# Kernel optimization log

Measured on AMD Instinct MI355X. Metric: run time of the kernel, lower is better.

The kernel has to match this reference:

```python
import jax, jax.numpy as jnp
import numpy as np

B = 16384   # tokens
K = 2       # top_k
E = 64      # num_experts
H = 512     # hidden_dim
F = 1024    # expert ffn dim


def setup_inputs() -> dict:
    key = jax.random.key(0)
    k1, k2, k3, k4, k5 = jax.random.split(key, 5)
    hidden_states = jax.random.normal(k1, (B, H), dtype=jnp.float32)
    expert_weights = jax.nn.softmax(jax.random.normal(k2, (B, K), dtype=jnp.float32), axis=-1)
    # Balanced routing: exactly B*K/E assignments per expert (random permutation
    # of a tiled pattern). This is a valid routing for the module and lets the
    # reference use a fixed-capacity grouped GEMM with zero token dropping.
    flat_ids = jax.random.permutation(k3, jnp.tile(jnp.arange(E, dtype=jnp.int32), (B * K) // E))
    expert_ids = flat_ids.reshape(B, K)
    W1 = jax.random.normal(k4, (E, H, F), dtype=jnp.float32) * (1.0 / np.sqrt(H))
    W2 = jax.random.normal(k5, (E, F, H), dtype=jnp.float32) * (1.0 / np.sqrt(F))
    return {"hidden_states": hidden_states, "expert_weights": expert_weights,
            "expert_ids": expert_ids, "W1": W1, "W2": W2}


def reference(hidden_states, expert_weights, expert_ids, W1, W2):
    # Faithful to ExpertGrouping.group_dispatch: every (token, slot) assignment
    # is run through its expert, scaled by its routing weight, and index_add'ed
    # back into the per-token output. Since assignments within an expert are
    # order-independent, we sort assignments by expert id and run one grouped
    # batched GEMM (the fused equivalent of the per-group/per-expert loops).
    b, h = hidden_states.shape
    k = expert_ids.shape[1]
    e = W1.shape[0]
    n = b * k
    cap = n // e  # exact per-expert count (balanced routing)

    flat_ids = expert_ids.reshape(-1)            # [N]
    flat_w = expert_weights.reshape(-1)          # [N]
    token_idx = jnp.arange(n, dtype=jnp.int32) // k  # [N] token for each assignment

    order = jnp.argsort(flat_ids)                # stable sort: groups assignments by expert
    tok_sorted = token_idx[order]                # [N]
    w_sorted = flat_w[order]                     # [N]

    # Gather-dispatch: [E, cap, H]
    xg = hidden_states[tok_sorted].reshape(e, cap, h)
    # Grouped expert FFN (batched over experts)
    hid = jax.nn.silu(jnp.einsum('ech,ehf->ecf', xg, W1))
    yg = jnp.einsum('ecf,efh->ech', hid, W2)     # [E, cap, H]

    # Weighted scatter-combine back to tokens
    weighted = yg.reshape(n, h) * w_sorted[:, None]
    out = jnp.zeros((b, h), dtype=hidden_states.dtype).at[tok_sorted].add(weighted)
    return out
```

## Files before the change

kernel.cpp:

```cpp
#include <hip/hip_runtime.h>
#include <hip/hip_bf16.h>

#define B_TOK 16384
#define TOPK 2
#define NEXP 64
#define HID 512
#define FFN 1024
#define NASSIGN (B_TOK * TOPK)
#define CAP (NASSIGN / NEXP)

typedef unsigned short u16;
typedef __bf16 bf16_t;
typedef bf16_t bf16x8 __attribute__((ext_vector_type(8)));
typedef float f32x4 __attribute__((ext_vector_type(4)));

__device__ __forceinline__ unsigned pkbf(float a, float b) {
  union { bf16_t h[2]; unsigned u; } v;
  v.h[0] = (bf16_t)a; v.h[1] = (bf16_t)b;
  return v.u;
}
__device__ __forceinline__ u16 f2bf(float f) {
  union { bf16_t h; u16 u; } v; v.h = (bf16_t)f; return v.u;
}
__device__ __forceinline__ float bf2f(unsigned u16v) {
  union { unsigned u; float f; } v; v.u = u16v << 16; return v.f;
}

#define GLOAD_LDS16(g, l)                                                     \
  __builtin_amdgcn_global_load_lds((const __attribute__((address_space(1))) void*)(g), \
                                   (__attribute__((address_space(3))) void*)(l), 16, 0, 0)

__global__ void k_route(const int* __restrict__ ids, int* __restrict__ cnt,
                        int* __restrict__ tok_of, int* __restrict__ slot_pos) {
  int n = blockIdx.x * blockDim.x + threadIdx.x;
  if (n >= NASSIGN) return;
  int e = ids[n];
  int r = atomicAdd(&cnt[e], 1);
  int p = e * CAP + r;
  tok_of[p] = n >> 1;
  slot_pos[n] = p;
}

__global__ void k_gather(const float* __restrict__ hs, const int* __restrict__ tok_of,
                         u16* __restrict__ Xg) {
  int p = blockIdx.x * 4 + (threadIdx.x >> 6);
  int lane = threadIdx.x & 63;
  const float4* src = reinterpret_cast<const float4*>(hs + (size_t)tok_of[p] * HID);
  uint2* dst = reinterpret_cast<uint2*>(Xg + (size_t)p * HID);
#pragma unroll
  for (int i = 0; i < 2; i++) {
    float4 v = src[i * 64 + lane];
    uint2 o;
    o.x = pkbf(v.x, v.y);
    o.y = pkbf(v.z, v.w);
    dst[i * 64 + lane] = o;
  }
}

template <int K, int NN, bool SILU>
__global__ __launch_bounds__(512, 2) void k_gemm(const u16* __restrict__ A,
                                                 const float* __restrict__ Wf,
                                                 u16* __restrict__ Cout) {
  constexpr int MT = CAP / 256;
  constexpr int NT = NN / 256;
  constexpr int NWG = NEXP * MT * NT;
  constexpr int Q = NWG / 8;
  constexpr int KT = K / 64;
  int wg = (blockIdx.x % 8) * Q + blockIdx.x / 8;
  int e = wg / (MT * NT);
  int rm = wg % (MT * NT);
  int mt = rm / NT, nt = rm % NT;

  const u16* Ab = A + ((size_t)e * CAP + (size_t)mt * 256) * K;

  __shared__ __align__(16) char smc[131072];

  int t_ = threadIdx.x;
  int lane = t_ & 63, wv = t_ >> 6;
  int wm = wv >> 2, wn = wv & 3;
  int l15 = lane & 15, lhi = lane >> 4;

  int srow = t_ >> 3;
  int gchunk = (t_ & 7) ^ (srow & 7);
  const u16* gA = Ab + (size_t)srow * K + gchunk * 8;
#define STAGE_HALF_A(tn, j)                                                  \
  do {                                                                       \
    char* d_ = smc + ((tn) & 1) * 32768 + (j) * 16384 + wv * 1024;           \
    const u16* s_ = gA + (size_t)((j) * 128) * K + (tn) * 64;                \
    GLOAD_LDS16(s_, d_);                                                     \
    GLOAD_LDS16(s_ + (size_t)64 * K, d_ + 8192);                             \
  } while (0)

  int kunit = t_ >> 6;
  int nunit = t_ & 63;
  const float* gWb = Wf + (size_t)e * K * NN + (size_t)(kunit * 8) * NN +
                     (size_t)nt * 256 + nunit * 4;
  int wbo[4];
#pragma unroll
  for (int i = 0; i < 4; i++) {
    int n = nunit * 4 + i;
    int S = (n ^ (n >> 3)) & 7;
    wbo[i] = n * 128 + ((kunit ^ S) << 4);
  }

  f32x4 acc[8][4];
#pragma unroll
  for (int i = 0; i < 8; i++)
#pragma unroll
    for (int j = 0; j < 4; j++) {
      f32x4 z = {0.f, 0.f, 0.f, 0.f};
      acc[i][j] = z;
    }
  bf16x8 a[4][2], b[4][2];

  int aof0 = (wm * 128 + l15) * 128 + ((lhi ^ (l15 & 7)) << 4);
  int aof1 = (wm * 128 + l15) * 128 + (((4 + lhi) ^ (l15 & 7)) << 4);
  int boff[4][2];
#pragma unroll
  for (int nf = 0; nf < 4; nf++) {
    int r = wn * 64 + nf * 16 + l15;
    int Sr = (r ^ (r >> 3)) & 7;
    boff[nf][0] = r * 128 + ((lhi ^ Sr) << 4);
    boff[nf][1] = r * 128 + (((4 + lhi) ^ Sr) << 4);
  }

#define BAR_THEN_LGKM0()                                                     \
  do {                                                                       \
    __builtin_amdgcn_sched_barrier(0);                                       \
    __builtin_amdgcn_s_barrier();                                            \
    asm volatile("s_waitcnt lgkmcnt(0)" ::: "memory");                       \
    __builtin_amdgcn_sched_barrier(0);                                       \
  } while (0)

#define MFMA_QUAD(mh, nh)                                                    \
  do {                                                                       \
    __builtin_amdgcn_s_setprio(1);                                           \
    _Pragma("unroll") for (int mf = 0; mf < 4; mf++)                         \
        _Pragma("unroll") for (int nf = 0; nf < 2; nf++)                     \
            _Pragma("unroll") for (int kk = 0; kk < 2; kk++)                 \
                acc[(mh)*4 + mf][(nh)*2 + nf] = __builtin_amdgcn_mfma_f32_16x16x32_bf16( \
                    a[mf][kk], b[(nh)*2 + nf][kk], acc[(mh)*4 + mf][(nh)*2 + nf], 0, 0, 0); \
    __builtin_amdgcn_s_setprio(0);                                           \
  } while (0)

  STAGE_HALF_A(0, 0); STAGE_HALF_A(0, 1);
  if (KT > 1) { STAGE_HALF_A(1, 0); STAGE_HALF_A(1, 1); }
  {
    float4 P[8];
#pragma unroll
    for (int j = 0; j < 8; j++)
      P[j] = *reinterpret_cast<const float4*>(gWb + (size_t)j * NN);
    char* wB = smc + 65536;
#pragma unroll
    for (int i = 0; i < 4; i++) {
      uint4 v;
      v.x = pkbf(P[0][i], P[1][i]); v.y = pkbf(P[2][i], P[3][i]);
      v.z = pkbf(P[4][i], P[5][i]); v.w = pkbf(P[6][i], P[7][i]);
      *reinterpret_cast<uint4*>(wB + wbo[i]) = v;
    }
  }
  asm volatile("s_waitcnt vmcnt(0) lgkmcnt(0)" ::: "memory");
  __builtin_amdgcn_sched_barrier(0);
  __builtin_amdgcn_s_barrier();

  for (int t = 0; t < KT; t++) {
    const char* pA = smc + (t & 1) * 32768;
    const char* pB = smc + 65536 + (t & 1) * 32768;
    char* wB = smc + 65536 + ((t + 1) & 1) * 32768;
    float4 L0, L1, L2, L3, L4, L5, L6, L7;

#pragma unroll
    for (int mf = 0; mf < 4; mf++) {
      a[mf][0] = *reinterpret_cast<const bf16x8*>(pA + aof0 + mf * 2048);
      a[mf][1] = *reinterpret_cast<const bf16x8*>(pA + aof1 + mf * 2048);
    }
#pragma unroll
    for (int nf = 0; nf < 2; nf++) {
      b[nf][0] = *reinterpret_cast<const bf16x8*>(pB + boff[nf][0]);
      b[nf][1] = *reinterpret_cast<const bf16x8*>(pB + boff[nf][1]);
    }
    if (t + 1 < KT) {
      const float* g = gWb + (size_t)(t + 1) * 64 * NN;
      L0 = *reinterpret_cast<const float4*>(g);
      L1 = *reinterpret_cast<const float4*>(g + (size_t)1 * NN);
      L2 = *reinterpret_cast<const float4*>(g + (size_t)2 * NN);
      L3 = *reinterpret_cast<const float4*>(g + (size_t)3 * NN);
    }
    BAR_THEN_LGKM0();
    MFMA_QUAD(0, 0);
    __builtin_amdgcn_s_barrier();

#pragma unroll
    for (int nf = 0; nf < 2; nf++) {
      b[2 + nf][0] = *reinterpret_cast<const bf16x8*>(pB + boff[2 + nf][0]);
      b[2 + nf][1] = *reinterpret_cast<const bf16x8*>(pB + boff[2 + nf][1]);
    }
    if (t + 1 < KT) {
      const float* g = gWb + (size_t)(t + 1) * 64 * NN;
      L4 = *reinterpret_cast<const float4*>(g + (size_t)4 * NN);
      L5 = *reinterpret_cast<const float4*>(g + (size_t)5 * NN);
      L6 = *reinterpret_cast<const float4*>(g + (size_t)6 * NN);
      L7 = *reinterpret_cast<const float4*>(g + (size_t)7 * NN);
    }
    BAR_THEN_LGKM0();
    MFMA_QUAD(0, 1);
    __builtin_amdgcn_s_barrier();

#pragma unroll
    for (int mf = 0; mf < 4; mf++) {
      a[mf][0] = *reinterpret_cast<const bf16x8*>(pA + aof0 + (4 + mf) * 2048);
      a[mf][1] = *reinterpret_cast<const bf16x8*>(pA + aof1 + (4 + mf) * 2048);
    }
    BAR_THEN_LGKM0();
    MFMA_QUAD(1, 0);
    __builtin_amdgcn_s_barrier();

    if (t + 2 < KT) { STAGE_HALF_A(t + 2, 0); STAGE_HALF_A(t + 2, 1); }
    if (t + 1 < KT) {
      if (t + 2 < KT)
        asm volatile("s_waitcnt vmcnt(4)" ::: "memory");
      else
        asm volatile("s_waitcnt vmcnt(0)" ::: "memory");
      __builtin_amdgcn_sched_barrier(0);
#pragma unroll
      for (int i = 0; i < 4; i++) {
        uint4 v;
        v.x = pkbf(L0[i], L1[i]); v.y = pkbf(L2[i], L3[i]);
        v.z = pkbf(L4[i], L5[i]); v.w = pkbf(L6[i], L7[i]);
        *reinterpret_cast<uint4*>(wB + wbo[i]) = v;
      }
    }
    BAR_THEN_LGKM0();
    MFMA_QUAD(1, 1);
    __builtin_amdgcn_s_barrier();
  }
#undef STAGE_HALF_A
#undef MFMA_QUAD
#undef BAR_THEN_LGKM0

#pragma unroll
  for (int mf = 0; mf < 8; mf++) {
#pragma unroll
    for (int nf = 0; nf < 4; nf++) {
#pragma unroll
      for (int rg = 0; rg < 4; rg++) {
        float v = acc[mf][nf][rg];
        int grow = mt * 256 + wm * 128 + mf * 16 + lhi * 4 + rg;
        int gcol = nt * 256 + wn * 64 + nf * 16 + l15;
        size_t off = ((size_t)e * CAP + grow) * NN + gcol;
        if constexpr (SILU) v = v / (1.0f + __expf(-v));
        Cout[off] = f2bf(v);
      }
    }
  }
}

__global__ void k_combine(const u16* __restrict__ yws, const int* __restrict__ slot_pos,
                          const float* __restrict__ w, float* __restrict__ out) {
  int tk = blockIdx.x * 4 + (threadIdx.x >> 6);
  int lane = threadIdx.x & 63;
  int p0 = slot_pos[2 * tk], p1 = slot_pos[2 * tk + 1];
  float w0 = w[2 * tk], w1 = w[2 * tk + 1];
  uint4 ua = reinterpret_cast<const uint4*>(yws + (size_t)p0 * HID)[lane];
  uint4 ub = reinterpret_cast<const uint4*>(yws + (size_t)p1 * HID)[lane];
  float4 o0, o1;
  o0.x = w0 * bf2f(ua.x & 0xffffu) + w1 * bf2f(ub.x & 0xffffu);
  o0.y = w0 * bf2f(ua.x >> 16) + w1 * bf2f(ub.x >> 16);
  o0.z = w0 * bf2f(ua.y & 0xffffu) + w1 * bf2f(ub.y & 0xffffu);
  o0.w = w0 * bf2f(ua.y >> 16) + w1 * bf2f(ub.y >> 16);
  o1.x = w0 * bf2f(ua.z & 0xffffu) + w1 * bf2f(ub.z & 0xffffu);
  o1.y = w0 * bf2f(ua.z >> 16) + w1 * bf2f(ub.z >> 16);
  o1.z = w0 * bf2f(ua.w & 0xffffu) + w1 * bf2f(ub.w & 0xffffu);
  o1.w = w0 * bf2f(ua.w >> 16) + w1 * bf2f(ub.w >> 16);
  float4* dst = reinterpret_cast<float4*>(out + (size_t)tk * HID + lane * 8);
  dst[0] = o0;
  dst[1] = o1;
}

extern "C" void kernel_launch(void* const* d_in, const int* in_sizes, int n_in,
                              void* d_out, int out_size, void* d_ws, size_t ws_size,
                              hipStream_t stream) {
  const float* hs = (const float*)d_in[0];
  const float* wts = (const float*)d_in[1];
  const int* ids = (const int*)d_in[2];
  const float* W1 = (const float*)d_in[3];
  const float* W2 = (const float*)d_in[4];
  float* out = (float*)d_out;

  char* ws = (char*)d_ws;
  size_t o = 0;
  int* cnt = (int*)(ws + o);       o += 1024;
  int* slot_pos = (int*)(ws + o);  o += (size_t)NASSIGN * 4;
  int* tok_of = (int*)(ws + o);    o += (size_t)NASSIGN * 4;
  o = (o + 255) & ~(size_t)255;
  u16* Xg = (u16*)(ws + o);        o += (size_t)NASSIGN * HID * 2;
  u16* hid = (u16*)(ws + o);       o += (size_t)NASSIGN * FFN * 2;
  u16* yws = (u16*)(ws + o);       o += (size_t)NASSIGN * HID * 2;

  hipMemsetAsync(cnt, 0, NEXP * sizeof(int), stream);
  k_route<<<(NASSIGN + 255) / 256, 256, 0, stream>>>(ids, cnt, tok_of, slot_pos);
  k_gather<<<NASSIGN / 4, 256, 0, stream>>>(hs, tok_of, Xg);
  k_gemm<HID, FFN, true><<<NEXP * (CAP / 256) * (FFN / 256), 512, 0, stream>>>(Xg, W1, hid);
  k_gemm<FFN, HID, false><<<NEXP * (CAP / 256) * (HID / 256), 512, 0, stream>>>(hid, W2, yws);
  k_combine<<<B_TOK / 4, 256, 0, stream>>>(yws, slot_pos, wts, out);
}
```

Before: 213.8 us.

## Collapse per-iteration barriers to one and issue A staging one tile ahead

Restructures the K-loop of the grouped GEMM: instead of four barrier-separated MFMA quarters per tile with A staged two tiles ahead, it issues all next-tile W loads and A async staging at the top, does all LDS reads and MFMA work for the current tile, then converts and stores B and places a single barrier at the end. The intent is to cut the synchronisation overhead and let waves drift apart to overlap MFMA with memory. In exchange, prefetch depth for A drops from two tiles to one, so global latency may be exposed, and barrier count falls from eight to one per iteration.

```diff
diff --git a/kernel.cpp b/kernel.cpp
--- a/kernel.cpp
+++ b/kernel.cpp
@@ -124,10 +124,8 @@
     boff[nf][1] = r * 128 + (((4 + lhi) ^ Sr) << 4);
   }
 
-#define BAR_THEN_LGKM0()                                                     \
+#define LGKM0()                                                              \
   do {                                                                       \
-    __builtin_amdgcn_sched_barrier(0);                                       \
-    __builtin_amdgcn_s_barrier();                                            \
     asm volatile("s_waitcnt lgkmcnt(0)" ::: "memory");                       \
     __builtin_amdgcn_sched_barrier(0);                                       \
   } while (0)
@@ -144,12 +142,13 @@
   } while (0)
 
   STAGE_HALF_A(0, 0); STAGE_HALF_A(0, 1);
-  if (KT > 1) { STAGE_HALF_A(1, 0); STAGE_HALF_A(1, 1); }
   {
     float4 P[8];
 #pragma unroll
     for (int j = 0; j < 8; j++)
       P[j] = *reinterpret_cast<const float4*>(gWb + (size_t)j * NN);
+    asm volatile("s_waitcnt vmcnt(0)" ::: "memory");
+    __builtin_amdgcn_sched_barrier(0);
     char* wB = smc + 65536;
 #pragma unroll
     for (int i = 0; i < 4; i++) {
@@ -159,8 +158,7 @@
       *reinterpret_cast<uint4*>(wB + wbo[i]) = v;
     }
   }
-  asm volatile("s_waitcnt vmcnt(0) lgkmcnt(0)" ::: "memory");
-  __builtin_amdgcn_sched_barrier(0);
+  LGKM0();
   __builtin_amdgcn_s_barrier();
 
   for (int t = 0; t < KT; t++) {
@@ -169,58 +167,44 @@
     char* wB = smc + 65536 + ((t + 1) & 1) * 32768;
     float4 L0, L1, L2, L3, L4, L5, L6, L7;
 
-#pragma unroll
-    for (int mf = 0; mf < 4; mf++) {
-      a[mf][0] = *reinterpret_cast<const bf16x8*>(pA + aof0 + mf * 2048);
-      a[mf][1] = *reinterpret_cast<const bf16x8*>(pA + aof1 + mf * 2048);
-    }
-#pragma unroll
-    for (int nf = 0; nf < 2; nf++) {
-      b[nf][0] = *reinterpret_cast<const bf16x8*>(pB + boff[nf][0]);
-      b[nf][1] = *reinterpret_cast<const bf16x8*>(pB + boff[nf][1]);
-    }
     if (t + 1 < KT) {
       const float* g = gWb + (size_t)(t + 1) * 64 * NN;
       L0 = *reinterpret_cast<const float4*>(g);
       L1 = *reinterpret_cast<const float4*>(g + (size_t)1 * NN);
       L2 = *reinterpret_cast<const float4*>(g + (size_t)2 * NN);
       L3 = *reinterpret_cast<const float4*>(g + (size_t)3 * NN);
-    }
-    BAR_THEN_LGKM0();
-    MFMA_QUAD(0, 0);
-    __builtin_amdgcn_s_barrier();
-
-#pragma unroll
-    for (int nf = 0; nf < 2; nf++) {
-      b[2 + nf][0] = *reinterpret_cast<const bf16x8*>(pB + boff[2 + nf][0]);
-      b[2 + nf][1] = *reinterpret_cast<const bf16x8*>(pB + boff[2 + nf][1]);
-    }
-    if (t + 1 < KT) {
-      const float* g = gWb + (size_t)(t + 1) * 64 * NN;
       L4 = *reinterpret_cast<const float4*>(g + (size_t)4 * NN);
       L5 = *reinterpret_cast<const float4*>(g + (size_t)5 * NN);
       L6 = *reinterpret_cast<const float4*>(g + (size_t)6 * NN);
       L7 = *reinterpret_cast<const float4*>(g + (size_t)7 * NN);
-    }
-    BAR_THEN_LGKM0();
+      STAGE_HALF_A(t + 1, 0); STAGE_HALF_A(t + 1, 1);
+    }
+
+#pragma unroll
+    for (int mf = 0; mf < 4; mf++) {
+      a[mf][0] = *reinterpret_cast<const bf16x8*>(pA + aof0 + mf * 2048);
+      a[mf][1] = *reinterpret_cast<const bf16x8*>(pA + aof1 + mf * 2048);
+    }
+#pragma unroll
+    for (int nf = 0; nf < 4; nf++) {
+      b[nf][0] = *reinterpret_cast<const bf16x8*>(pB + boff[nf][0]);
+      b[nf][1] = *reinterpret_cast<const bf16x8*>(pB + boff[nf][1]);
+    }
+    LGKM0();
+    MFMA_QUAD(0, 0);
     MFMA_QUAD(0, 1);
-    __builtin_amdgcn_s_barrier();
 
 #pragma unroll
     for (int mf = 0; mf < 4; mf++) {
       a[mf][0] = *reinterpret_cast<const bf16x8*>(pA + aof0 + (4 + mf) * 2048);
       a[mf][1] = *reinterpret_cast<const bf16x8*>(pA + aof1 + (4 + mf) * 2048);
     }
-    BAR_THEN_LGKM0();
+    LGKM0();
     MFMA_QUAD(1, 0);
-    __builtin_amdgcn_s_barrier();
-
-    if (t + 2 < KT) { STAGE_HALF_A(t + 2, 0); STAGE_HALF_A(t + 2, 1); }
+    MFMA_QUAD(1, 1);
+
     if (t + 1 < KT) {
-      if (t + 2 < KT)
-        asm volatile("s_waitcnt vmcnt(4)" ::: "memory");
-      else
-        asm volatile("s_waitcnt vmcnt(0)" ::: "memory");
+      asm volatile("s_waitcnt vmcnt(4)" ::: "memory");
       __builtin_amdgcn_sched_barrier(0);
 #pragma unroll
       for (int i = 0; i < 4; i++) {
@@ -229,14 +213,14 @@
         v.z = pkbf(L4[i], L5[i]); v.w = pkbf(L6[i], L7[i]);
         *reinterpret_cast<uint4*>(wB + wbo[i]) = v;
       }
-    }
-    BAR_THEN_LGKM0();
-    MFMA_QUAD(1, 1);
-    __builtin_amdgcn_s_barrier();
+      asm volatile("s_waitcnt vmcnt(0) lgkmcnt(0)" ::: "memory");
+      __builtin_amdgcn_sched_barrier(0);
+      __builtin_amdgcn_s_barrier();
+    }
   }
 #undef STAGE_HALF_A
 #undef MFMA_QUAD
-#undef BAR_THEN_LGKM0
+#undef LGKM0
 
 #pragma unroll
   for (int mf = 0; mf < 8; mf++) {
```

After: 206.7 us (median of 3 runs). -3.3%, faster.
